# Kernel optimization log

Measured on AMD Instinct MI355X. Metric: run time of the kernel, lower is better.

Reference implementation:

```python
import jax, jax.numpy as jnp
import numpy as np

D_MODEL = 1024
NUM_HEADS = 16
HEAD_DIM = D_MODEL // NUM_HEADS
BATCH = 8
SEQ = 2048
LN_EPS = 1e-5


def setup_inputs() -> dict:
    rng = jax.random.key(0)
    ks = jax.random.split(rng, 16)
    s = 0.02  # init scale for weights
    w = lambda k: jax.random.normal(k, (D_MODEL, D_MODEL), jnp.float32) * s
    return {
        "query": jax.random.normal(ks[0], (BATCH, SEQ, D_MODEL), jnp.float32),
        "key": jax.random.normal(ks[1], (BATCH, SEQ, D_MODEL), jnp.float32),
        "value": jax.random.normal(ks[2], (BATCH, SEQ, D_MODEL), jnp.float32),
        "Wq": w(ks[3]), "bq": jnp.zeros((D_MODEL,), jnp.float32),
        "Wk": w(ks[4]), "bk": jnp.zeros((D_MODEL,), jnp.float32),
        "Wv": w(ks[5]), "bv": jnp.zeros((D_MODEL,), jnp.float32),
        "ln_g": jnp.ones((D_MODEL,), jnp.float32),
        "ln_b": jnp.zeros((D_MODEL,), jnp.float32),
        "Wo": w(ks[6]), "bo": jnp.zeros((D_MODEL,), jnp.float32),
    }


def reference(query, key, value, Wq, bq, Wk, bk, Wv, bv, ln_g, ln_b, Wo, bo):
    N, L, dm = query.shape
    H, Dh = NUM_HEADS, HEAD_DIM
    # projections + split heads -> (N, H, L, Dh), matching torch .view().transpose(1,2)
    q = (query @ Wq.T + bq).reshape(N, L, H, Dh).transpose(0, 2, 1, 3)
    k = (key   @ Wk.T + bk).reshape(N, L, H, Dh).transpose(0, 2, 1, 3)
    v = (value @ Wv.T + bv).reshape(N, L, H, Dh).transpose(0, 2, 1, 3)
    # Faithful to source: einsum 'nqhd,nkhd->nhqk' applied to ALREADY-transposed
    # (N,H,L,Dh) tensors => per-position head-to-head attention, energy (N, L, H, H).
    energy = jnp.einsum('nhld,ngld->nlhg', q, k)  # (N, L, H, H)
    attn = jax.nn.softmax(energy / jnp.sqrt(jnp.float32(dm)), axis=3)
    # source einsum 'nhql,nlhd->nqhd' on transposed v -> (N, H, L, Dh)
    out = jnp.einsum('nlhg,ngld->nhld', attn, v)
    out = out.transpose(0, 2, 1, 3).reshape(N, L, dm)
    # dropout is identity in eval mode
    mu = out.mean(axis=-1, keepdims=True)
    var = out.var(axis=-1, keepdims=True)
    out = (out - mu) / jnp.sqrt(var + LN_EPS) * ln_g + ln_b
    return out @ Wo.T + bo
```

## Files before the change

### kernel.cpp

```cpp
#include <hip/hip_runtime.h>
#include <cstdint>

#define TOKENS 16384
#define DMODEL 1024
#define NHEADS 16
#define HDIM   64

typedef __bf16  bf16x8 __attribute__((ext_vector_type(8)));
typedef ushort  u16x8  __attribute__((ext_vector_type(8)));
typedef ushort  u16x4  __attribute__((ext_vector_type(4)));
typedef float   f32x4  __attribute__((ext_vector_type(4)));

__device__ __forceinline__ ushort f2bf(float f) {
    union { float f; unsigned int i; } v; v.f = f;
    return (ushort)((v.i + 0x8000u) >> 16);
}
__device__ __forceinline__ f32x4 mfma16(bf16x8 a, bf16x8 b, f32x4 c) {
    return __builtin_amdgcn_mfma_f32_16x16x32_bf16(a, b, c, 0, 0, 0);
}
__device__ __forceinline__ void gload_lds16(const void* g, void* l) {
    __builtin_amdgcn_global_load_lds(
        (const __attribute__((address_space(1))) unsigned int*)(uintptr_t)g,
        (__attribute__((address_space(3))) unsigned int*)(uintptr_t)l,
        16, 0, 0);
}
union BU { u16x8 u; bf16x8 b; };

struct CvtArgs {
    const float* src[4];
    ushort*      dst[4];
};

__global__ __launch_bounds__(256) void cvt_f32_bf16(CvtArgs a)
{
    const float* __restrict__ s = a.src[blockIdx.y];
    ushort*      __restrict__ d = a.dst[blockIdx.y];
    const long i = ((long)blockIdx.x * 256 + threadIdx.x) * 8;
    const f32x4 v0 = *(const f32x4*)(s + i);
    const f32x4 v1 = *(const f32x4*)(s + i + 4);
    u16x8 p;
    #pragma unroll
    for (int j = 0; j < 4; j++) {
        p[j]     = f2bf(v0[j]);
        p[4 + j] = f2bf(v1[j]);
    }
    *(u16x8*)(d + i) = p;
}

#define BM2 256
#define BN2 256
#define BK2 32

struct GemmArgs {
    const ushort* A[3];
    const ushort* W[3];
    const float*  Bi[3];
    void*         C[3];
};

#define G256_READ_B(slot)                                                     \
    { _Pragma("unroll")                                                       \
      for (int n = 0; n < 4; ++n)                                             \
          bf[n] = *(const bf16x8*)&Bs[slot][(wn * 64 + n * 16 + fr) * BK2 + fks]; }

#define G256_READ_A(slot, mh)                                                 \
    { _Pragma("unroll")                                                       \
      for (int m = 0; m < 4; ++m)                                             \
          af[m] = *(const bf16x8*)&As[slot][(wm * 128 + (mh) * 64 + m * 16 + fr) * BK2 + fks]; }

#define G256_MFMA(mh)                                                         \
    { __builtin_amdgcn_s_setprio(1);                                          \
      _Pragma("unroll")                                                       \
      for (int m = 0; m < 4; ++m)                                             \
          _Pragma("unroll")                                                   \
          for (int n = 0; n < 4; ++n)                                         \
              acc[(mh) * 4 + m][n] = mfma16(af[m], bf[n], acc[(mh) * 4 + m][n]); \
      __builtin_amdgcn_s_setprio(0); }

template<int BF16OUT>
__global__ __launch_bounds__(512) void gemm256(GemmArgs args, int N, int K)
{
    __shared__ __align__(16) ushort As[4][BM2 * BK2];
    __shared__ __align__(16) ushort Bs[4][BN2 * BK2];

    const int gx = gridDim.x, gy = gridDim.y;
    const int lin = (blockIdx.z * gy + blockIdx.y) * gx + blockIdx.x;
    const int nwg = gx * gy * gridDim.z;
    const int q = nwg >> 3, r = nwg & 7;
    const int xcd = lin & 7, loc = lin >> 3;
    const int swz = (xcd < r ? xcd * (q + 1) : r * (q + 1) + (xcd - r) * q) + loc;
    const int bz  = swz / (gx * gy);
    const int rem = swz - bz * gx * gy;
    const int by  = rem / gx;
    const int bx  = rem - by * gx;

    const ushort* __restrict__ A  = args.A[bz];
    const ushort* __restrict__ W  = args.W[bz];
    const float*  __restrict__ Bi = args.Bi[bz];

    const int tid  = threadIdx.x;
    const int wave = tid >> 6;
    const int lane = tid & 63;
    const int wm = wave >> 2;
    const int wn = wave & 3;
    const long rowBase = (long)by * BM2;
    const long colBase = (long)bx * BN2;

    const int gA0 = tid, gA1 = tid + 512;
    const long aOff0 = (long)(gA0 >> 2) * K + (((gA0 & 3) ^ ((gA0 >> 3) & 3)) * 8);
    const long aOff1 = (long)(gA1 >> 2) * K + (((gA1 & 3) ^ ((gA1 >> 3) & 3)) * 8);
    const ushort* Abase = A + rowBase * K;
    const ushort* Wbase = W + colBase * K;

    const int fr  = lane & 15;
    const int fks = (((lane >> 4) ^ ((fr >> 1) & 3)) * 8);

    f32x4 acc[8][4];
    #pragma unroll
    for (int m = 0; m < 8; ++m)
        #pragma unroll
        for (int n = 0; n < 4; ++n)
            acc[m][n] = (f32x4){0.f, 0.f, 0.f, 0.f};

    auto stageA = [&](int slot, int kt) {
        gload_lds16(Abase + aOff0 + (long)kt * BK2, &As[slot][gA0 * 8]);
        gload_lds16(Abase + aOff1 + (long)kt * BK2, &As[slot][gA1 * 8]);
    };
    auto stageB = [&](int slot, int kt) {
        gload_lds16(Wbase + aOff0 + (long)kt * BK2, &Bs[slot][gA0 * 8]);
        gload_lds16(Wbase + aOff1 + (long)kt * BK2, &Bs[slot][gA1 * 8]);
    };

    const int nt = K / BK2;

    stageA(0, 0); stageB(0, 0);
    stageA(1, 1); stageB(1, 1);
    stageA(2, 2); stageB(2, 2);
    asm volatile("s_waitcnt vmcnt(8)" ::: "memory");
    __builtin_amdgcn_s_barrier();

    bf16x8 af[4], bf[4];

    for (int X = 0; X < nt - 3; ++X) {
        const int slot = X & 3, st = (X + 3) & 3;
        G256_READ_B(slot);
        G256_READ_A(slot, 0);
        stageA(st, X + 3);
        G256_MFMA(0);
        __builtin_amdgcn_s_barrier();
        G256_READ_A(slot, 1);
        stageB(st, X + 3);
        G256_MFMA(1);
        asm volatile("s_waitcnt vmcnt(8)" ::: "memory");
        __builtin_amdgcn_s_barrier();
    }
    {
        const int slot = (nt - 3) & 3;
        G256_READ_B(slot);
        G256_READ_A(slot, 0);
        G256_MFMA(0);
        __builtin_amdgcn_s_barrier();
        G256_READ_A(slot, 1);
        G256_MFMA(1);
        asm volatile("s_waitcnt vmcnt(4)" ::: "memory");
        __builtin_amdgcn_s_barrier();
    }
    {
        const int slot = (nt - 2) & 3;
        G256_READ_B(slot);
        G256_READ_A(slot, 0);
        G256_MFMA(0);
        __builtin_amdgcn_s_barrier();
        G256_READ_A(slot, 1);
        G256_MFMA(1);
        asm volatile("s_waitcnt vmcnt(0)" ::: "memory");
        __builtin_amdgcn_s_barrier();
    }
    {
        const int slot = (nt - 1) & 3;
        G256_READ_B(slot);
        G256_READ_A(slot, 0);
        G256_MFMA(0);
        __builtin_amdgcn_s_barrier();
        G256_READ_A(slot, 1);
        G256_MFMA(1);
    }

    const int qd = lane >> 4;
    #pragma unroll
    for (int n = 0; n < 4; ++n) {
        const long col = colBase + wn * 64 + n * 16 + fr;
        const float bv = Bi[col];
        #pragma unroll
        for (int m = 0; m < 8; ++m) {
            const long r0 = rowBase + wm * 128 + m * 16 + qd * 4;
            #pragma unroll
            for (int r2 = 0; r2 < 4; ++r2) {
                const float val = acc[m][n][r2] + bv;
                if (BF16OUT)
                    ((ushort*)args.C[bz])[(r0 + r2) * (long)N + col] = f2bf(val);
                else
                    ((float*)args.C[bz])[(r0 + r2) * (long)N + col] = val;
            }
        }
    }
}

#define PMS 40

__global__ __launch_bounds__(256) void attn_ln_mfma(
    const ushort* __restrict__ Qp, const ushort* __restrict__ Kp,
    const ushort* __restrict__ Vp,
    const float* __restrict__ lng, const float* __restrict__ lnb,
    ushort* __restrict__ O)
{
    __shared__ __align__(16) ushort Vs[4][16 * 64];
    __shared__ __align__(16) ushort Pm[4][16 * PMS];

    const int tid  = threadIdx.x;
    const int w    = tid >> 6;
    const int lane = tid & 63;
    const long tok  = (long)blockIdx.x * 4 + w;
    const long base = tok * DMODEL;

    gload_lds16(Vp + base +       lane * 8, &Vs[w][      lane * 8]);
    gload_lds16(Vp + base + 512 + lane * 8, &Vs[w][512 + lane * 8]);

    *(u16x4*)&Pm[w][(lane & 15) * PMS + 16 + (lane >> 4) * 4] = (u16x4){0, 0, 0, 0};

    const int fr = lane & 15;
    const int fs = (lane >> 4) * 8;

    const bf16x8 aq0 = *(const bf16x8*)(Qp + base + fr * 64 + fs);
    const bf16x8 aq1 = *(const bf16x8*)(Qp + base + fr * 64 + fs + 32);
    const bf16x8 bk0 = *(const bf16x8*)(Kp + base + fr * 64 + fs);
    const bf16x8 bk1 = *(const bf16x8*)(Kp + base + fr * 64 + fs + 32);

    f32x4 e = (f32x4){0.f, 0.f, 0.f, 0.f};
    e = mfma16(aq0, bk0, e);
    e = mfma16(aq1, bk1, e);

    #pragma unroll
    for (int r = 0; r < 4; ++r) {
        const float x = e[r] * 0.03125f;
        float mx = x;
        #pragma unroll
        for (int m = 1; m < 16; m <<= 1) mx = fmaxf(mx, __shfl_xor(mx, m, 64));
        const float ex = __expf(x - mx);
        float sm = ex;
        #pragma unroll
        for (int m = 1; m < 16; m <<= 1) sm += __shfl_xor(sm, m, 64);
        Pm[w][((lane >> 4) * 4 + r) * PMS + fr] = f2bf(ex / sm);
    }

    __syncthreads();

    const bf16x8 pa = *(const bf16x8*)&Pm[w][fr * PMS + fs];

    f32x4 o[4];
    #pragma unroll
    for (int dblk = 0; dblk < 4; ++dblk) {
        BU bu; bu.u = (u16x8){0, 0, 0, 0, 0, 0, 0, 0};
        if (lane < 32) {
            #pragma unroll
            for (int j = 0; j < 8; ++j)
                bu.u[j] = Vs[w][(fs + j) * 64 + dblk * 16 + fr];
        }
        o[dblk] = mfma16(pa, bu.b, (f32x4){0.f, 0.f, 0.f, 0.f});
    }

    float s1 = 0.f, s2 = 0.f;
    #pragma unroll
    for (int dblk = 0; dblk < 4; ++dblk)
        #pragma unroll
        for (int r = 0; r < 4; ++r) { const float v = o[dblk][r]; s1 += v; s2 += v * v; }
    #pragma unroll
    for (int m = 1; m < 64; m <<= 1) {
        s1 += __shfl_xor(s1, m, 64);
        s2 += __shfl_xor(s2, m, 64);
    }
    const float mu   = s1 * (1.f / DMODEL);
    const float var  = s2 * (1.f / DMODEL) - mu * mu;
    const float rstd = rsqrtf(var + 1e-5f);

    #pragma unroll
    for (int dblk = 0; dblk < 4; ++dblk) {
        #pragma unroll
        for (int r = 0; r < 4; ++r) {
            const int h = (lane >> 4) * 4 + r;
            const int i = h * HDIM + dblk * 16 + fr;
            O[base + i] = f2bf((o[dblk][r] - mu) * rstd * lng[i] + lnb[i]);
        }
    }
}

extern "C" void kernel_launch(void* const* d_in, const int* in_sizes, int n_in,
                              void* d_out, int out_size, void* d_ws, size_t ws_size,
                              hipStream_t stream)
{
    const float* query = (const float*)d_in[0];
    const float* key   = (const float*)d_in[1];
    const float* value = (const float*)d_in[2];
    const float* Wq = (const float*)d_in[3];
    const float* bq = (const float*)d_in[4];
    const float* Wk = (const float*)d_in[5];
    const float* bk = (const float*)d_in[6];
    const float* Wv = (const float*)d_in[7];
    const float* bv = (const float*)d_in[8];
    const float* lng = (const float*)d_in[9];
    const float* lnb = (const float*)d_in[10];
    const float* Wo = (const float*)d_in[11];
    const float* bo = (const float*)d_in[12];
    float* out = (float*)d_out;

    const long WELEMS = (long)DMODEL * DMODEL;

    ushort* wq_b = (ushort*)d_ws;
    ushort* wk_b = wq_b + WELEMS;
    ushort* wv_b = wk_b + WELEMS;
    ushort* wo_b = wv_b + WELEMS;
    ushort* cbuf = wo_b + WELEMS;

    int NC = 1;
    while (NC < 64 &&
           (size_t)(8 * WELEMS) + (size_t)(TOKENS / NC) * DMODEL * 10 > ws_size)
        NC <<= 1;
    const int CM = TOKENS / NC;
    const size_t CE = (size_t)CM * DMODEL;

    ushort* qb = cbuf;
    ushort* kb = qb + CE;
    ushort* vb = kb + CE;
    ushort* qp = vb + CE;
    ushort* vp = qp + CE;

    {
        CvtArgs cw;
        cw.src[0] = Wq; cw.src[1] = Wk; cw.src[2] = Wv; cw.src[3] = Wo;
        cw.dst[0] = wq_b; cw.dst[1] = wk_b; cw.dst[2] = wv_b; cw.dst[3] = wo_b;
        cvt_f32_bf16<<<dim3((unsigned)(WELEMS / 2048), 4), 256, 0, stream>>>(cw);
    }

    for (int c = 0; c < NC; ++c) {
        const size_t off = (size_t)c * CE;
        ushort* kp = (ushort*)(out + off);

        {
            CvtArgs ci;
            ci.src[0] = query + off; ci.src[1] = key + off; ci.src[2] = value + off;
            ci.src[3] = query;
            ci.dst[0] = qb; ci.dst[1] = kb; ci.dst[2] = vb; ci.dst[3] = qb;
            cvt_f32_bf16<<<dim3((unsigned)(CE / 2048), 3), 256, 0, stream>>>(ci);
        }

        GemmArgs g1;
        g1.A[0] = qb;    g1.A[1] = kb;   g1.A[2] = vb;
        g1.W[0] = wq_b;  g1.W[1] = wk_b; g1.W[2] = wv_b;
        g1.Bi[0] = bq;   g1.Bi[1] = bk;  g1.Bi[2] = bv;
        g1.C[0] = qp;    g1.C[1] = kp;   g1.C[2] = vp;
        gemm256<1><<<dim3(DMODEL / BN2, CM / BM2, 3), 512, 0, stream>>>(
            g1, DMODEL, DMODEL);

        attn_ln_mfma<<<CM / 4, 256, 0, stream>>>(qp, kp, vp, lng, lnb, qb);

        GemmArgs g2;
        g2.A[0] = g2.A[1] = g2.A[2] = qb;
        g2.W[0] = g2.W[1] = g2.W[2] = wo_b;
        g2.Bi[0] = g2.Bi[1] = g2.Bi[2] = bo;
        g2.C[0] = g2.C[1] = g2.C[2] = out + off;
        gemm256<0><<<dim3(DMODEL / BN2, CM / BM2, 1), 512, 0, stream>>>(
            g2, DMODEL, DMODEL);
    }
}
```

Measured before the change: 432.0 us.

## Rework head-attention kernel: transposed energy MFMA, K16 PV, swizzled V, vectorized LN store

Swaps the operands of the energy MFMA so each lane holds a full softmax row across 4 registers. This cuts the shuffle reductions and removes the LDS round trip for P when the 16x16x16 bf16 MFMA builtin is available. V is loaded into LDS with an XOR swizzle to reduce bank conflicts, and __syncthreads is replaced by a per-wave vmcnt wait. The LayerNorm output is staged through LDS so each lane writes 16 contiguous bf16 values with vector stores. The trade-off is extra LDS use and a preprocessor-dependent code path.

```diff
diff --git a/kernel.cpp b/kernel.cpp
--- a/kernel.cpp
+++ b/kernel.cpp
@@ -9,7 +9,14 @@
 typedef __bf16  bf16x8 __attribute__((ext_vector_type(8)));
 typedef ushort  u16x8  __attribute__((ext_vector_type(8)));
 typedef ushort  u16x4  __attribute__((ext_vector_type(4)));
+typedef short   s16x4  __attribute__((ext_vector_type(4)));
 typedef float   f32x4  __attribute__((ext_vector_type(4)));
+
+#if defined(__has_builtin)
+#if __has_builtin(__builtin_amdgcn_mfma_f32_16x16x16bf16_1k)
+#define HAVE_MFMA_K16 1
+#endif
+#endif
 
 __device__ __forceinline__ ushort f2bf(float f) {
     union { float f; unsigned int i; } v; v.f = f;
@@ -214,8 +221,13 @@
     const float* __restrict__ lng, const float* __restrict__ lnb,
     ushort* __restrict__ O)
 {
-    __shared__ __align__(16) ushort Vs[4][16 * 64];
+#if HAVE_MFMA_K16
+    __shared__ __align__(16) ushort Vs[4][1024];
+#else
+    __shared__ __align__(16) ushort Vs[4][2048];
     __shared__ __align__(16) ushort Pm[4][16 * PMS];
+#endif
+    __shared__ __align__(16) float Os[4][16 * 68];
 
     const int tid  = threadIdx.x;
     const int w    = tid >> 6;
@@ -223,13 +235,17 @@
     const long tok  = (long)blockIdx.x * 4 + w;
     const long base = tok * DMODEL;
 
-    gload_lds16(Vp + base +       lane * 8, &Vs[w][      lane * 8]);
-    gload_lds16(Vp + base + 512 + lane * 8, &Vs[w][512 + lane * 8]);
-
-    *(u16x4*)&Pm[w][(lane & 15) * PMS + 16 + (lane >> 4) * 4] = (u16x4){0, 0, 0, 0};
+    {
+        const int i0 = lane, i1 = lane + 64;
+        const int g0 = i0 >> 3, d80 = (i0 & 7) ^ (((i0 >> 5) & 3) << 1);
+        const int g1 = i1 >> 3, d81 = (i1 & 7) ^ (((i1 >> 5) & 3) << 1);
+        gload_lds16(Vp + base + g0 * 64 + d80 * 8, &Vs[w][i0 * 8]);
+        gload_lds16(Vp + base + g1 * 64 + d81 * 8, &Vs[w][i1 * 8]);
+    }
 
     const int fr = lane & 15;
-    const int fs = (lane >> 4) * 8;
+    const int hi = lane >> 4;
+    const int fs = hi * 8;
 
     const bf16x8 aq0 = *(const bf16x8*)(Qp + base + fr * 64 + fs);
     const bf16x8 aq1 = *(const bf16x8*)(Qp + base + fr * 64 + fs + 32);
@@ -237,37 +253,68 @@
     const bf16x8 bk1 = *(const bf16x8*)(Kp + base + fr * 64 + fs + 32);
 
     f32x4 e = (f32x4){0.f, 0.f, 0.f, 0.f};
-    e = mfma16(aq0, bk0, e);
-    e = mfma16(aq1, bk1, e);
-
-    #pragma unroll
-    for (int r = 0; r < 4; ++r) {
-        const float x = e[r] * 0.03125f;
-        float mx = x;
-        #pragma unroll
-        for (int m = 1; m < 16; m <<= 1) mx = fmaxf(mx, __shfl_xor(mx, m, 64));
-        const float ex = __expf(x - mx);
-        float sm = ex;
-        #pragma unroll
-        for (int m = 1; m < 16; m <<= 1) sm += __shfl_xor(sm, m, 64);
-        Pm[w][((lane >> 4) * 4 + r) * PMS + fr] = f2bf(ex / sm);
-    }
-
-    __syncthreads();
-
-    const bf16x8 pa = *(const bf16x8*)&Pm[w][fr * PMS + fs];
+    e = mfma16(bk0, aq0, e);
+    e = mfma16(bk1, aq1, e);
+
+    float x[4];
+    #pragma unroll
+    for (int r = 0; r < 4; ++r) x[r] = e[r] * 0.03125f;
+    float mx = fmaxf(fmaxf(x[0], x[1]), fmaxf(x[2], x[3]));
+    mx = fmaxf(mx, __shfl_xor(mx, 16, 64));
+    mx = fmaxf(mx, __shfl_xor(mx, 32, 64));
+    float ex[4], sm;
+    #pragma unroll
+    for (int r = 0; r < 4; ++r) ex[r] = __expf(x[r] - mx);
+    sm = (ex[0] + ex[1]) + (ex[2] + ex[3]);
+    sm += __shfl_xor(sm, 16, 64);
+    sm += __shfl_xor(sm, 32, 64);
+    const float inv = 1.0f / sm;
+    float p[4];
+    #pragma unroll
+    for (int r = 0; r < 4; ++r) p[r] = ex[r] * inv;
 
     f32x4 o[4];
+
+#if HAVE_MFMA_K16
+    s16x4 pa;
+    #pragma unroll
+    for (int r = 0; r < 4; ++r) pa[r] = (short)f2bf(p[r]);
+
+    asm volatile("s_waitcnt vmcnt(0)" ::: "memory");
+
     #pragma unroll
     for (int dblk = 0; dblk < 4; ++dblk) {
-        BU bu; bu.u = (u16x8){0, 0, 0, 0, 0, 0, 0, 0};
-        if (lane < 32) {
-            #pragma unroll
-            for (int j = 0; j < 8; ++j)
-                bu.u[j] = Vs[w][(fs + j) * 64 + dblk * 16 + fr];
+        s16x4 bv;
+        #pragma unroll
+        for (int j = 0; j < 4; ++j) {
+            const int g = hi * 4 + j;
+            const int d = dblk * 16 + fr;
+            const int ad = g * 64 + (((d >> 3) ^ (((g >> 2) & 3) << 1)) * 8) + (d & 7);
+            bv[j] = (short)Vs[w][ad];
         }
-        o[dblk] = mfma16(pa, bu.b, (f32x4){0.f, 0.f, 0.f, 0.f});
-    }
+        o[dblk] = __builtin_amdgcn_mfma_f32_16x16x16bf16_1k(
+            pa, bv, (f32x4){0.f, 0.f, 0.f, 0.f}, 0, 0, 0);
+    }
+#else
+    *(u16x4*)&Pm[w][fr * PMS + 16 + hi * 4] = (u16x4){0, 0, 0, 0};
+    #pragma unroll
+    for (int r = 0; r < 4; ++r)
+        Pm[w][fr * PMS + hi * 4 + r] = f2bf(p[r]);
+    asm volatile("s_waitcnt vmcnt(0)" ::: "memory");
+    const bf16x8 pa8 = *(const bf16x8*)&Pm[w][fr * PMS + fs];
+    #pragma unroll
+    for (int dblk = 0; dblk < 4; ++dblk) {
+        BU bu;
+        #pragma unroll
+        for (int j = 0; j < 8; ++j) {
+            const int g = fs + j;
+            const int d = dblk * 16 + fr;
+            const int ad = g * 64 + (((d >> 3) ^ (((g >> 2) & 3) << 1)) * 8) + (d & 7);
+            bu.u[j] = Vs[w][ad];
+        }
+        o[dblk] = mfma16(pa8, bu.b, (f32x4){0.f, 0.f, 0.f, 0.f});
+    }
+#endif
 
     float s1 = 0.f, s2 = 0.f;
     #pragma unroll
@@ -284,14 +331,25 @@
     const float rstd = rsqrtf(var + 1e-5f);
 
     #pragma unroll
-    for (int dblk = 0; dblk < 4; ++dblk) {
-        #pragma unroll
-        for (int r = 0; r < 4; ++r) {
-            const int h = (lane >> 4) * 4 + r;
-            const int i = h * HDIM + dblk * 16 + fr;
-            O[base + i] = f2bf((o[dblk][r] - mu) * rstd * lng[i] + lnb[i]);
+    for (int dblk = 0; dblk < 4; ++dblk)
+        #pragma unroll
+        for (int r = 0; r < 4; ++r)
+            Os[w][(hi * 4 + r) * 68 + dblk * 16 + fr] = (o[dblk][r] - mu) * rstd;
+
+    u16x8 s0, s1v;
+    #pragma unroll
+    for (int c = 0; c < 4; ++c) {
+        const f32x4 yv = *(const f32x4*)&Os[w][(lane >> 2) * 68 + (lane & 3) * 16 + c * 4];
+        const f32x4 lg = *(const f32x4*)(lng + lane * 16 + c * 4);
+        const f32x4 lb = *(const f32x4*)(lnb + lane * 16 + c * 4);
+        #pragma unroll
+        for (int j = 0; j < 4; ++j) {
+            const ushort hv = f2bf(yv[j] * lg[j] + lb[j]);
+            if (c < 2) s0[c * 4 + j] = hv; else s1v[(c - 2) * 4 + j] = hv;
         }
     }
+    *(u16x8*)(O + base + lane * 16)     = s0;
+    *(u16x8*)(O + base + lane * 16 + 8) = s1v;
 }
 
 extern "C" void kernel_launch(void* const* d_in, const int* in_sizes, int n_in,
```

Result: no change. 433.6 us (+0.4%).
